# Performance work log

Hardware: AMD Instinct MI355X
Metric: run time of the kernel (lower is better)

Reference implementation:

```python
import jax, jax.numpy as jnp
import numpy as np

NUM_HEADS = 12
WINDOW = 128
LOOK_B = 1
LOOK_F = 1


def look_around(x, pad_value):
    # x: (b, n_windows, window, ...) ; pad along window axis (axis=1), concat along axis=2
    pads = [(0, 0), (LOOK_B, LOOK_F)] + [(0, 0)] * (x.ndim - 2)
    p = jnp.pad(x, pads, constant_values=pad_value)
    n = x.shape[1]
    return jnp.concatenate([p[:, i:i + n] for i in range(LOOK_B + LOOK_F + 1)], axis=2)


def split_heads(x):
    # (L, B, D) -> (B*H, L, hd), batch-major over heads (index = b*H + h)
    L, B, D = x.shape
    return jnp.transpose(x.reshape(L, B * NUM_HEADS, D // NUM_HEADS), (1, 0, 2))


def merge_heads(x):
    # (B*H, L, hd) -> (L, B, D)
    BH, L, hd = x.shape
    return jnp.transpose(x, (1, 0, 2)).reshape(L, BH // NUM_HEADS, hd * NUM_HEADS)


def setup_inputs() -> dict:
    key = jax.random.key(0)
    ks = jax.random.split(key, 12)
    S, B, D = 4096, 8, 768
    inp = {
        'hidden_states': jax.random.normal(ks[0], (S, B, D), dtype=jnp.float32),
        'key_padding_mask': jax.random.bernoulli(ks[1], 0.2, (B, S)),
    }
    scale = 0.02
    for i, name in enumerate(['Wq', 'Wk', 'Wv', 'Wgq']):
        inp[name] = jax.random.normal(ks[2 + i], (D, D), dtype=jnp.float32) * scale
    for i, name in enumerate(['bq', 'bk', 'bv', 'bgq']):
        inp[name] = jax.random.normal(ks[6 + i], (D,), dtype=jnp.float32) * scale
    return inp


def reference(hidden_states, key_padding_mask, Wq, bq, Wk, bk, Wv, bv, Wgq, bgq):
    S, B, D = hidden_states.shape
    H, W = NUM_HEADS, WINDOW
    hd = D // H
    n = S // W
    BH = B * H
    neg = -jnp.finfo(hidden_states.dtype).max
    inv_sqrt = hd ** (-0.5)

    q = split_heads(hidden_states @ Wq + bq)  # (BH, S, hd)
    k = split_heads(hidden_states @ Wk + bk)
    v = split_heads(hidden_states @ Wv + bv)

    # --- local windowed attention ---
    bq_ = q.reshape(BH, n, W, hd)
    bk_ = look_around(k.reshape(BH, n, W, hd), 0.0)   # (BH, n, 3W, hd)
    bv_ = look_around(v.reshape(BH, n, W, hd), 0.0)
    dots = jnp.einsum('bnie,bnje->bnij', bq_, bk_) * inv_sqrt  # (BH, n, W, 3W)

    im = key_padding_mask.reshape(B, n, W)
    km = look_around(im, True)                        # (B, n, 3W), pads masked
    mask = im[:, :, :, None] | km[:, :, None, :]      # (B, n, W, 3W)
    mask = jnp.broadcast_to(mask[:, None], (B, H, n, W, 3 * W)).reshape(BH, n, W, 3 * W)
    dots = jnp.where(mask, neg, dots)
    attn = jax.nn.softmax(dots, axis=-1)
    out = jnp.einsum('bnij,bnje->bnie', attn, bv_).reshape(BH, S, hd)
    out = merge_heads(out)                            # (S, B, D)

    # --- global-token attention (token 0 attends to everything) ---
    gq = split_heads(hidden_states[0:1] @ Wgq + bgq)  # (BH, 1, hd)
    gdots = jnp.einsum('bie,bje->bij', gq, k) * inv_sqrt  # (BH, 1, S)
    gmask = jnp.broadcast_to(key_padding_mask[:, None], (B, H, S)).reshape(BH, S)
    gdots = jnp.where(gmask[:, None, :], neg, gdots)
    gattn = jax.nn.softmax(gdots, axis=-1)
    gout = merge_heads(jnp.einsum('bij,bje->bie', gattn, v))  # (1, B, D)

    return out.at[0].set(gout[0])
```

## Files before the change

### kernel.cpp

```cpp
#include <hip/hip_runtime.h>
#include <float.h>

#define S_  4096
#define B_  8
#define D_  768
#define H_  12
#define HD_ 64
#define W_  128
#define BH_ 96
#define SB_ 32768

typedef unsigned short u16;
typedef __attribute__((ext_vector_type(8))) short bf16x8;
typedef __attribute__((ext_vector_type(4))) float f32x4;

#define MFMA16(a,b,c) __builtin_amdgcn_mfma_f32_16x16x32_bf16(a,b,c,0,0,0)

__device__ __forceinline__ u16 f2bf(float x){
  unsigned int u = __float_as_uint(x);
  return (u16)((u + 0x7FFFu + ((u >> 16) & 1u)) >> 16);
}
__device__ __forceinline__ float bf2f(unsigned int lo16){ return __uint_as_float(lo16 << 16); }
__device__ __forceinline__ float bflo(unsigned int u){ return __uint_as_float(u << 16); }
__device__ __forceinline__ float bfhi(unsigned int u){ return __uint_as_float(u & 0xFFFF0000u); }
__device__ __forceinline__ unsigned int pk2(float a, float b){
  return (unsigned int)f2bf(a) | ((unsigned int)f2bf(b) << 16);
}

__device__ __forceinline__ bool mask_at(const void* mp, int flag, int idx){
  return flag ? (((const unsigned char*)mp)[idx] != 0)
              : (((const unsigned int*)mp)[idx] != 0u);
}

__global__ __launch_bounds__(256) void sniff_mask_kernel(const unsigned int* __restrict__ m,
                                                         int* __restrict__ flag){
  __shared__ unsigned int red[256];
  unsigned int acc = 0u;
  for (int i = threadIdx.x; i < 8192; i += 256) acc |= m[i];
  red[threadIdx.x] = acc;
  __syncthreads();
  for (int s = 128; s > 0; s >>= 1){
    if ((int)threadIdx.x < s) red[threadIdx.x] |= red[threadIdx.x + s];
    __syncthreads();
  }
  if (threadIdx.x == 0){
    unsigned int o = red[0];
    *flag = (o > 1u && (o & 0xFEFEFEFEu) == 0u) ? 1 : 0;
  }
}

__global__ __launch_bounds__(256) void cvt_hidden_kernel(const float* __restrict__ src,
                                                         u16* __restrict__ dst){
  int idx = blockIdx.x * 256 + threadIdx.x;
  for (int base = idx * 8; base < 25165824; base += 2048 * 256 * 8){
    float4 a = *(const float4*)&src[base];
    float4 b = *(const float4*)&src[base + 4];
    uint4 o;
    o.x = pk2(a.x, a.y); o.y = pk2(a.z, a.w);
    o.z = pk2(b.x, b.y); o.w = pk2(b.z, b.w);
    *(uint4*)&dst[base] = o;
  }
}

__global__ __launch_bounds__(256) void cvt_wT_kernel(const float* __restrict__ W0,
    const float* __restrict__ W1, const float* __restrict__ W2, u16* __restrict__ wT){
  __shared__ float tile[64][65];
  const float* Wsel = blockIdx.z == 0 ? W0 : (blockIdx.z == 1 ? W1 : W2);
  const int t = threadIdx.x;
  const int kt0 = blockIdx.x * 64, nt0 = blockIdx.y * 64;
  { const int row = t >> 2, c16 = (t & 3) * 16;
#pragma unroll
    for (int j = 0; j < 4; ++j){
      float4 v = *(const float4*)&Wsel[(size_t)(kt0 + row) * 768 + nt0 + c16 + j * 4];
      tile[row][c16 + j*4 + 0] = v.x; tile[row][c16 + j*4 + 1] = v.y;
      tile[row][c16 + j*4 + 2] = v.z; tile[row][c16 + j*4 + 3] = v.w;
    } }
  __syncthreads();
  { const int nl = t >> 2, k16 = (t & 3) * 16;
    unsigned int o[8];
#pragma unroll
    for (int j = 0; j < 8; ++j)
      o[j] = pk2(tile[k16 + 2*j][nl], tile[k16 + 2*j + 1][nl]);
    u16* dst = wT + (size_t)blockIdx.z * 589824 + (size_t)(nt0 + nl) * 768 + kt0 + k16;
    *(uint4*)dst       = make_uint4(o[0], o[1], o[2], o[3]);
    *(uint4*)(dst + 8) = make_uint4(o[4], o[5], o[6], o[7]); }
}

__global__ __launch_bounds__(256) void proj_mfma_kernel(
    const u16* __restrict__ hb, const u16* __restrict__ wT,
    const float* __restrict__ bq, const float* __restrict__ bk, const float* __restrict__ bv,
    u16* __restrict__ qb, u16* __restrict__ kb, u16* __restrict__ vb){
  __shared__ u16 As[128][72];
  __shared__ u16 Bs[128][72];
  const int t = threadIdx.x;
  const int p  = blockIdx.y / 6;
  const int c0 = (blockIdx.y % 6) * 128;
  const int r0 = blockIdx.x * 128;
  const float* bias = p == 0 ? bq : (p == 1 ? bk : bv);
  u16* dst = p == 0 ? qb : (p == 1 ? kb : vb);
  const u16* wTp = wT + (size_t)p * 589824;

  const int lane = t & 63, w = t >> 6;
  const int l15 = lane & 15, lg = lane >> 4;
  const int wr = w >> 1, wc = w & 1;

  f32x4 acc[4][4] = {};

  for (int k0 = 0; k0 < 768; k0 += 64){
#pragma unroll
    for (int i = 0; i < 4; ++i){
      int chunk = i * 256 + t;
      int row = chunk >> 3, q8 = (chunk & 7) * 8;
      *(uint4*)&As[row][q8] = *(const uint4*)&hb[(size_t)(r0 + row) * 768 + k0 + q8];
      *(uint4*)&Bs[row][q8] = *(const uint4*)&wTp[(size_t)(c0 + row) * 768 + k0 + q8];
    }
    __syncthreads();
    bf16x8 af[4][2], bf[4][2];
#pragma unroll
    for (int mf = 0; mf < 4; ++mf)
#pragma unroll
      for (int ks = 0; ks < 2; ++ks)
        af[mf][ks] = *(const bf16x8*)&As[wr*64 + mf*16 + l15][ks*32 + lg*8];
#pragma unroll
    for (int nf = 0; nf < 4; ++nf)
#pragma unroll
      for (int ks = 0; ks < 2; ++ks)
        bf[nf][ks] = *(const bf16x8*)&Bs[wc*64 + nf*16 + l15][ks*32 + lg*8];
#pragma unroll
    for (int ks = 0; ks < 2; ++ks)
#pragma unroll
      for (int mf = 0; mf < 4; ++mf)
#pragma unroll
        for (int nf = 0; nf < 4; ++nf)
          acc[mf][nf] = MFMA16(af[mf][ks], bf[nf][ks], acc[mf][nf]);
    __syncthreads();
  }
#pragma unroll
  for (int nf = 0; nf < 4; ++nf){
    int c = c0 + wc*64 + nf*16 + l15;
    float bsv = bias[c];
    int hh = c >> 6, dd = c & 63;
#pragma unroll
    for (int mf = 0; mf < 4; ++mf){
      int rbase = r0 + wr*64 + mf*16 + lg*4;
#pragma unroll
      for (int r = 0; r < 4; ++r){
        int row = rbase + r;
        int s = row >> 3, b = row & 7;
        dst[((size_t)(b * 12 + hh) * 4096 + s) * 64 + dd] = f2bf(acc[mf][nf][r] + bsv);
      }
    }
  }
}

__global__ __launch_bounds__(256) void vt_kernel(const u16* __restrict__ vb, u16* __restrict__ vtb){
  __shared__ u16 tile[64][72];
  const int t = threadIdx.x;
  const int stile = blockIdx.x, bh = blockIdx.y;
  { const int sl = t >> 2, q = (t & 3) * 16;
    const u16* src = &vb[((size_t)bh * 4096 + stile * 64 + sl) * 64 + q];
    *(uint4*)&tile[sl][q]     = *(const uint4*)src;
    *(uint4*)&tile[sl][q + 8] = *(const uint4*)(src + 8); }
  __syncthreads();
  { const int d = t >> 2, sq = (t & 3) * 16;
    unsigned int o[8];
#pragma unroll
    for (int j = 0; j < 8; ++j){
      unsigned int lo = tile[sq + 2*j][d], hi = tile[sq + 2*j + 1][d];
      o[j] = lo | (hi << 16);
    }
    u16* dst = vtb + ((size_t)bh * 64 + d) * 4096 + stile * 64 + sq;
    *(uint4*)dst       = make_uint4(o[0], o[1], o[2], o[3]);
    *(uint4*)(dst + 8) = make_uint4(o[4], o[5], o[6], o[7]); }
}

__global__ __launch_bounds__(256) void local_mfma_kernel(
    const u16* __restrict__ qb, const u16* __restrict__ kb, const u16* __restrict__ vtb,
    const void* __restrict__ maskp, const int* __restrict__ flagp,
    float* __restrict__ out){
  __shared__ u16 Ks[64][72];
  __shared__ u16 Vs[64][72];
  __shared__ u16 Ps[4][32][72];
  __shared__ float kpen[384];
  __shared__ float qpen_s[128];
  const int t = threadIdx.x;
  const int n_i = blockIdx.x, bh = blockIdx.y;
  const int b_i = bh / 12, h = bh % 12;
  const int flag = *flagp;
  const int w = t >> 6, lane = t & 63, l15 = lane & 15, lg = lane >> 4;
  const int jbase0 = n_i * 128 - 128;

  if (t < 128) qpen_s[t] = mask_at(maskp, flag, b_i * 4096 + n_i * 128 + t) ? 1.f : 0.f;
  for (int j = t; j < 384; j += 256){
    int jp = jbase0 + j;
    kpen[j] = (jp < 0 || jp >= 4096 || mask_at(maskp, flag, b_i * 4096 + jp)) ? 1.f : 0.f;
  }
  __syncthreads();

  bf16x8 aq[2][2];
#pragma unroll
  for (int mf = 0; mf < 2; ++mf)
#pragma unroll
    for (int ks = 0; ks < 2; ++ks)
      aq[mf][ks] = *(const bf16x8*)&qb[((size_t)bh * 4096 + n_i*128 + w*32 + mf*16 + l15) * 64 + ks*32 + lg*8];

  float qp[2][4];
#pragma unroll
  for (int mf = 0; mf < 2; ++mf)
#pragma unroll
    for (int r = 0; r < 4; ++r)
      qp[mf][r] = qpen_s[w*32 + mf*16 + lg*4 + r];

  f32x4 O[2][4] = {};
  float mrow[2][4], lrow[2][4];
#pragma unroll
  for (int mf = 0; mf < 2; ++mf)
#pragma unroll
    for (int r = 0; r < 4; ++r){ mrow[mf][r] = -FLT_MAX; lrow[mf][r] = 0.f; }

  for (int jt = 0; jt < 6; ++jt){
    const int jb = jbase0 + jt * 64;
    if (jb < 0 || jb >= 4096) continue;
#pragma unroll
    for (int i = 0; i < 2; ++i){
      int chunk = i * 256 + t;
      int row = chunk >> 3, q8 = (chunk & 7) * 8;
      *(uint4*)&Ks[row][q8] = *(const uint4*)&kb[((size_t)bh * 4096 + jb + row) * 64 + q8];
      *(uint4*)&Vs[row][q8] = *(const uint4*)&vtb[((size_t)bh * 64 + row) * 4096 + jb + q8];
    }
    __syncthreads();

    f32x4 dt[2][4] = {};
#pragma unroll
    for (int ks = 0; ks < 2; ++ks)
#pragma unroll
      for (int nf = 0; nf < 4; ++nf){
        bf16x8 bk_ = *(const bf16x8*)&Ks[nf*16 + l15][ks*32 + lg*8];
        dt[0][nf] = MFMA16(aq[0][ks], bk_, dt[0][nf]);
        dt[1][nf] = MFMA16(aq[1][ks], bk_, dt[1][nf]);
      }
#pragma unroll
    for (int nf = 0; nf < 4; ++nf){
      float kp = kpen[jt*64 + nf*16 + l15];
#pragma unroll
      for (int mf = 0; mf < 2; ++mf)
#pragma unroll
        for (int r = 0; r < 4; ++r){
          float vv = dt[mf][nf][r] * 0.125f;
          dt[mf][nf][r] = (qp[mf][r] + kp == 0.f) ? vv : -FLT_MAX;
        }
    }
#pragma unroll
    for (int mf = 0; mf < 2; ++mf)
#pragma unroll
      for (int r = 0; r < 4; ++r){
        float tm = fmaxf(fmaxf(dt[mf][0][r], dt[mf][1][r]), fmaxf(dt[mf][2][r], dt[mf][3][r]));
        tm = fmaxf(tm, __shfl_xor(tm, 1));
        tm = fmaxf(tm, __shfl_xor(tm, 2));
        tm = fmaxf(tm, __shfl_xor(tm, 4));
        tm = fmaxf(tm, __shfl_xor(tm, 8));
        float mold = mrow[mf][r];
        float mnew = fmaxf(mold, tm);
        float scl = __expf(mold - mnew);
        mrow[mf][r] = mnew;
        float ps = 0.f;
#pragma unroll
        for (int nf = 0; nf < 4; ++nf){
          float pv = __expf(dt[mf][nf][r] - mnew);
          ps += pv;
          Ps[w][mf*16 + lg*4 + r][nf*16 + l15] = f2bf(pv);
          O[mf][nf][r] *= scl;
        }
        ps += __shfl_xor(ps, 1);
        ps += __shfl_xor(ps, 2);
        ps += __shfl_xor(ps, 4);
        ps += __shfl_xor(ps, 8);
        lrow[mf][r] = lrow[mf][r] * scl + ps;
      }
#pragma unroll
    for (int ks = 0; ks < 2; ++ks){
      bf16x8 ap0 = *(const bf16x8*)&Ps[w][l15]     [ks*32 + lg*8];
      bf16x8 ap1 = *(const bf16x8*)&Ps[w][16 + l15][ks*32 + lg*8];
#pragma unroll
      for (int nf = 0; nf < 4; ++nf){
        bf16x8 bv_ = *(const bf16x8*)&Vs[nf*16 + l15][ks*32 + lg*8];
        O[0][nf] = MFMA16(ap0, bv_, O[0][nf]);
        O[1][nf] = MFMA16(ap1, bv_, O[1][nf]);
      }
    }
    __syncthreads();
  }

  const float noor = (n_i == 0 || n_i == 31) ? 128.f : 0.f;
#pragma unroll
  for (int mf = 0; mf < 2; ++mf)
#pragma unroll
    for (int r = 0; r < 4; ++r){
      float lf = lrow[mf][r] + ((mrow[mf][r] <= -FLT_MAX) ? noor : 0.f);
      float inv = 1.f / lf;
      int srow = n_i*128 + w*32 + mf*16 + lg*4 + r;
      float* op = &out[(size_t)srow * (8 * 768) + b_i * 768 + h * 64];
#pragma unroll
      for (int nf = 0; nf < 4; ++nf)
        op[nf*16 + l15] = O[mf][nf][r] * inv;
    }
}

__global__ __launch_bounds__(256) void gq_kernel(const float* __restrict__ hid,
    const float* __restrict__ Wgq, const float* __restrict__ bgq, float* __restrict__ gq){
  __shared__ float hs[768];
  __shared__ float red[256];
  const int t = threadIdx.x, bh = blockIdx.x, b_i = bh / 12, h = bh % 12;
  for (int c = t; c < 768; c += 256) hs[c] = hid[(size_t)b_i * 768 + c];
  __syncthreads();
  const int dd = t & 63, part = t >> 6;
  float acc = 0.f;
  for (int c = part * 192; c < part * 192 + 192; ++c)
    acc += hs[c] * Wgq[(size_t)c * 768 + h * 64 + dd];
  red[t] = acc;
  __syncthreads();
  if (t < 64)
    gq[bh * 64 + t] = (red[t] + red[t+64] + red[t+128] + red[t+192] + bgq[h*64 + t]) * 0.125f;
}

__global__ __launch_bounds__(256) void gpart_kernel(const float* __restrict__ gq,
    const u16* __restrict__ kb, const u16* __restrict__ vb,
    const void* __restrict__ maskp, const int* __restrict__ flagp,
    float* __restrict__ gp_out){
  __shared__ float gqs[64];
  __shared__ float sc[512];
  __shared__ float red[256];
  const int t = threadIdx.x, bh = blockIdx.x, chunk = blockIdx.y;
  const int b_i = bh / 12;
  const int flag = *flagp;
  if (t < 64) gqs[t] = gq[bh * 64 + t];
  __syncthreads();
#pragma unroll
  for (int i = 0; i < 2; ++i){
    int sl = i * 256 + t;
    int s = chunk * 512 + sl;
    const uint4* kr = (const uint4*)&kb[((size_t)bh * 4096 + s) * 64];
    float dot = 0.f;
#pragma unroll
    for (int u = 0; u < 8; ++u){
      uint4 x = kr[u];
      dot += gqs[u*8+0]*bflo(x.x) + gqs[u*8+1]*bfhi(x.x);
      dot += gqs[u*8+2]*bflo(x.y) + gqs[u*8+3]*bfhi(x.y);
      dot += gqs[u*8+4]*bflo(x.z) + gqs[u*8+5]*bfhi(x.z);
      dot += gqs[u*8+6]*bflo(x.w) + gqs[u*8+7]*bfhi(x.w);
    }
    sc[sl] = mask_at(maskp, flag, b_i * 4096 + s) ? -FLT_MAX : dot;
  }
  __syncthreads();
  float m = fmaxf(sc[t], sc[t + 256]);
  red[t] = m; __syncthreads();
  for (int st = 128; st > 0; st >>= 1){ if (t < st) red[t] = fmaxf(red[t], red[t + st]); __syncthreads(); }
  const float mc = red[0];
  __syncthreads();
  float ls = 0.f;
#pragma unroll
  for (int i = 0; i < 2; ++i){
    int sl = i * 256 + t;
    float p = __expf(sc[sl] - mc);
    sc[sl] = p; ls += p;
  }
  red[t] = ls; __syncthreads();
  for (int st = 128; st > 0; st >>= 1){ if (t < st) red[t] += red[t + st]; __syncthreads(); }
  const float lc = red[0];
  __syncthreads();
  const int dd = t & 63, part = t >> 6;
  float o = 0.f;
  for (int i2 = 0; i2 < 128; ++i2){
    int sl = part * 128 + i2;
    o += sc[sl] * bf2f(vb[((size_t)bh * 4096 + chunk * 512 + sl) * 64 + dd]);
  }
  red[t] = o; __syncthreads();
  float* gp = gp_out + ((size_t)bh * 8 + chunk) * 66;
  if (t == 0){ gp[0] = mc; gp[1] = lc; }
  if (t < 64) gp[2 + t] = red[t] + red[t+64] + red[t+128] + red[t+192];
}

__global__ __launch_bounds__(64) void greduce_kernel(const float* __restrict__ gp_in,
                                                     float* __restrict__ out){
  const int t = threadIdx.x, bh = blockIdx.x, b_i = bh / 12, h = bh % 12;
  const float* gp = gp_in + (size_t)bh * 8 * 66;
  float mg = -FLT_MAX;
#pragma unroll
  for (int c = 0; c < 8; ++c) mg = fmaxf(mg, gp[c * 66]);
  float lg = 0.f, o = 0.f;
#pragma unroll
  for (int c = 0; c < 8; ++c){
    float wv = __expf(gp[c * 66] - mg);
    lg += gp[c * 66 + 1] * wv;
    o  += gp[c * 66 + 2 + t] * wv;
  }
  out[(size_t)b_i * 768 + h * 64 + t] = o / lg;
}

extern "C" void kernel_launch(void* const* d_in, const int* in_sizes, int n_in,
                              void* d_out, int out_size, void* d_ws, size_t ws_size,
                              hipStream_t stream) {
  const float* hid   = (const float*)d_in[0];
  const void*  maskp = d_in[1];
  const float* Wq  = (const float*)d_in[2];
  const float* Wk  = (const float*)d_in[3];
  const float* Wv  = (const float*)d_in[4];
  const float* Wgq = (const float*)d_in[5];
  const float* bq  = (const float*)d_in[6];
  const float* bk  = (const float*)d_in[7];
  const float* bv  = (const float*)d_in[8];
  const float* bgq = (const float*)d_in[9];
  float* out = (float*)d_out;

  char* wsb = (char*)d_ws;
  int* flag   = (int*)wsb;
  u16* hb     = (u16*)(wsb + 256);
  u16* wT     = (u16*)(wsb + 50331904);
  u16* qb     = (u16*)(wsb + 53870848);
  u16* kb     = (u16*)(wsb + 104202496);
  u16* vb     = (u16*)(wsb + 154534144);
  u16* vtb    = (u16*)(wsb + 204865792);
  float* gq   = (float*)(wsb + 255197440);
  float* gpart = (float*)(wsb + 255222016);

  sniff_mask_kernel<<<1, 256, 0, stream>>>((const unsigned int*)maskp, flag);
  cvt_hidden_kernel<<<2048, 256, 0, stream>>>(hid, hb);
  cvt_wT_kernel<<<dim3(12, 12, 3), 256, 0, stream>>>(Wq, Wk, Wv, wT);
  proj_mfma_kernel<<<dim3(256, 18), 256, 0, stream>>>(hb, wT, bq, bk, bv, qb, kb, vb);
  vt_kernel<<<dim3(64, 96), 256, 0, stream>>>(vb, vtb);
  gq_kernel<<<96, 256, 0, stream>>>(hid, Wgq, bgq, gq);
  local_mfma_kernel<<<dim3(32, 96), 256, 0, stream>>>(qb, kb, vtb, maskp, flag, out);
  gpart_kernel<<<dim3(96, 8), 256, 0, stream>>>(gq, kb, vb, maskp, flag, gpart);
  greduce_kernel<<<96, 64, 0, stream>>>(gpart, out);
}
```

Baseline: 431.2 us.

## Use direct global-to-LDS loads with XOR swizzle, XCD block remap, and MFMA priority

In the projection GEMM and the local attention kernel, global-to-LDS tile staging now goes through global_load_lds, which skips the round trip through registers. The padded shared-memory arrays are replaced by unpadded tiles with an XOR swizzle on the 16-byte slot index to avoid bank conflicts. The launch grid is flattened and block IDs are remapped so that consecutive IDs (id&7) are spread across the chiplet XCDs, aiming for better L2 locality. s_setprio is raised around the MFMA sections of the attention loop. The swizzle indexing has to match exactly between the writes and the reads, and the LDS-direct loads depend on each wave's lane-to-address layout.

```diff
diff --git a/kernel.cpp b/kernel.cpp
--- a/kernel.cpp
+++ b/kernel.cpp
@@ -25,6 +25,12 @@
 __device__ __forceinline__ float bfhi(unsigned int u){ return __uint_as_float(u & 0xFFFF0000u); }
 __device__ __forceinline__ unsigned int pk2(float a, float b){
   return (unsigned int)f2bf(a) | ((unsigned int)f2bf(b) << 16);
+}
+
+__device__ __forceinline__ void gload_lds16(const void* g, void* l){
+  __builtin_amdgcn_global_load_lds(
+      (const __attribute__((address_space(1))) void*)g,
+      (__attribute__((address_space(3))) void*)l, 16, 0, 0);
 }
 
 __device__ __forceinline__ bool mask_at(const void* mp, int flag, int idx){
@@ -90,12 +96,15 @@
     const u16* __restrict__ hb, const u16* __restrict__ wT,
     const float* __restrict__ bq, const float* __restrict__ bk, const float* __restrict__ bv,
     u16* __restrict__ qb, u16* __restrict__ kb, u16* __restrict__ vb){
-  __shared__ u16 As[128][72];
-  __shared__ u16 Bs[128][72];
+  __shared__ u16 As[128 * 64];
+  __shared__ u16 Bs[128 * 64];
   const int t = threadIdx.x;
-  const int p  = blockIdx.y / 6;
-  const int c0 = (blockIdx.y % 6) * 128;
-  const int r0 = blockIdx.x * 128;
+  const int id = blockIdx.x;
+  const int swz = (id & 7) * 576 + (id >> 3);
+  const int mt = swz & 255, nt = swz >> 8;
+  const int p  = nt / 6;
+  const int c0 = (nt % 6) * 128;
+  const int r0 = mt * 128;
   const float* bias = p == 0 ? bq : (p == 1 ? bk : bv);
   u16* dst = p == 0 ? qb : (p == 1 ? kb : vb);
   const u16* wTp = wT + (size_t)p * 589824;
@@ -103,16 +112,18 @@
   const int lane = t & 63, w = t >> 6;
   const int l15 = lane & 15, lg = lane >> 4;
   const int wr = w >> 1, wc = w & 1;
+  const int lrc = lane >> 3, slot = lane & 7;
 
   f32x4 acc[4][4] = {};
 
   for (int k0 = 0; k0 < 768; k0 += 64){
 #pragma unroll
-    for (int i = 0; i < 4; ++i){
-      int chunk = i * 256 + t;
-      int row = chunk >> 3, q8 = (chunk & 7) * 8;
-      *(uint4*)&As[row][q8] = *(const uint4*)&hb[(size_t)(r0 + row) * 768 + k0 + q8];
-      *(uint4*)&Bs[row][q8] = *(const uint4*)&wTp[(size_t)(c0 + row) * 768 + k0 + q8];
+    for (int c = 0; c < 4; ++c){
+      int chunk = w * 4 + c;
+      int ldsrow = chunk * 8 + lrc;
+      int slotg = slot ^ (ldsrow & 7);
+      gload_lds16(&hb [(size_t)(r0 + ldsrow) * 768 + k0 + slotg * 8], &As[chunk * 512]);
+      gload_lds16(&wTp[(size_t)(c0 + ldsrow) * 768 + k0 + slotg * 8], &Bs[chunk * 512]);
     }
     __syncthreads();
     bf16x8 af[4][2], bf[4][2];
@@ -120,12 +131,12 @@
     for (int mf = 0; mf < 4; ++mf)
 #pragma unroll
       for (int ks = 0; ks < 2; ++ks)
-        af[mf][ks] = *(const bf16x8*)&As[wr*64 + mf*16 + l15][ks*32 + lg*8];
+        af[mf][ks] = *(const bf16x8*)&As[(wr*64 + mf*16 + l15) * 64 + (((ks*4 + lg) ^ (l15 & 7)) * 8)];
 #pragma unroll
     for (int nf = 0; nf < 4; ++nf)
 #pragma unroll
       for (int ks = 0; ks < 2; ++ks)
-        bf[nf][ks] = *(const bf16x8*)&Bs[wc*64 + nf*16 + l15][ks*32 + lg*8];
+        bf[nf][ks] = *(const bf16x8*)&Bs[(wc*64 + nf*16 + l15) * 64 + (((ks*4 + lg) ^ (l15 & 7)) * 8)];
 #pragma unroll
     for (int ks = 0; ks < 2; ++ks)
 #pragma unroll
@@ -178,16 +189,19 @@
     const u16* __restrict__ qb, const u16* __restrict__ kb, const u16* __restrict__ vtb,
     const void* __restrict__ maskp, const int* __restrict__ flagp,
     float* __restrict__ out){
-  __shared__ u16 Ks[64][72];
-  __shared__ u16 Vs[64][72];
+  __shared__ u16 Ks[64 * 64];
+  __shared__ u16 Vs[64 * 64];
   __shared__ u16 Ps[4][32][72];
   __shared__ float kpen[384];
   __shared__ float qpen_s[128];
   const int t = threadIdx.x;
-  const int n_i = blockIdx.x, bh = blockIdx.y;
+  const int id = blockIdx.x;
+  const int swz = (id & 7) * 384 + (id >> 3);
+  const int n_i = swz & 31, bh = swz >> 5;
   const int b_i = bh / 12, h = bh % 12;
   const int flag = *flagp;
   const int w = t >> 6, lane = t & 63, l15 = lane & 15, lg = lane >> 4;
+  const int lrc = lane >> 3, slot = lane & 7;
   const int jbase0 = n_i * 128 - 128;
 
   if (t < 128) qpen_s[t] = mask_at(maskp, flag, b_i * 4096 + n_i * 128 + t) ? 1.f : 0.f;
@@ -222,23 +236,26 @@
     const int jb = jbase0 + jt * 64;
     if (jb < 0 || jb >= 4096) continue;
 #pragma unroll
-    for (int i = 0; i < 2; ++i){
-      int chunk = i * 256 + t;
-      int row = chunk >> 3, q8 = (chunk & 7) * 8;
-      *(uint4*)&Ks[row][q8] = *(const uint4*)&kb[((size_t)bh * 4096 + jb + row) * 64 + q8];
-      *(uint4*)&Vs[row][q8] = *(const uint4*)&vtb[((size_t)bh * 64 + row) * 4096 + jb + q8];
+    for (int c = 0; c < 2; ++c){
+      int chunk = w * 2 + c;
+      int ldsrow = chunk * 8 + lrc;
+      int slotg = slot ^ (ldsrow & 7);
+      gload_lds16(&kb [((size_t)bh * 4096 + jb + ldsrow) * 64 + slotg * 8], &Ks[chunk * 512]);
+      gload_lds16(&vtb[((size_t)bh * 64 + ldsrow) * 4096 + jb + slotg * 8], &Vs[chunk * 512]);
     }
     __syncthreads();
 
     f32x4 dt[2][4] = {};
+    __builtin_amdgcn_s_setprio(1);
 #pragma unroll
     for (int ks = 0; ks < 2; ++ks)
 #pragma unroll
       for (int nf = 0; nf < 4; ++nf){
-        bf16x8 bk_ = *(const bf16x8*)&Ks[nf*16 + l15][ks*32 + lg*8];
+        bf16x8 bk_ = *(const bf16x8*)&Ks[(nf*16 + l15) * 64 + (((ks*4 + lg) ^ (l15 & 7)) * 8)];
         dt[0][nf] = MFMA16(aq[0][ks], bk_, dt[0][nf]);
         dt[1][nf] = MFMA16(aq[1][ks], bk_, dt[1][nf]);
       }
+    __builtin_amdgcn_s_setprio(0);
 #pragma unroll
     for (int nf = 0; nf < 4; ++nf){
       float kp = kpen[jt*64 + nf*16 + l15];
@@ -277,17 +294,19 @@
         ps += __shfl_xor(ps, 8);
         lrow[mf][r] = lrow[mf][r] * scl + ps;
       }
+    __builtin_amdgcn_s_setprio(1);
 #pragma unroll
     for (int ks = 0; ks < 2; ++ks){
       bf16x8 ap0 = *(const bf16x8*)&Ps[w][l15]     [ks*32 + lg*8];
       bf16x8 ap1 = *(const bf16x8*)&Ps[w][16 + l15][ks*32 + lg*8];
 #pragma unroll
       for (int nf = 0; nf < 4; ++nf){
-        bf16x8 bv_ = *(const bf16x8*)&Vs[nf*16 + l15][ks*32 + lg*8];
+        bf16x8 bv_ = *(const bf16x8*)&Vs[(nf*16 + l15) * 64 + (((ks*4 + lg) ^ (l15 & 7)) * 8)];
         O[0][nf] = MFMA16(ap0, bv_, O[0][nf]);
         O[1][nf] = MFMA16(ap1, bv_, O[1][nf]);
       }
     }
+    __builtin_amdgcn_s_setprio(0);
     __syncthreads();
   }
 
@@ -426,10 +445,10 @@
   sniff_mask_kernel<<<1, 256, 0, stream>>>((const unsigned int*)maskp, flag);
   cvt_hidden_kernel<<<2048, 256, 0, stream>>>(hid, hb);
   cvt_wT_kernel<<<dim3(12, 12, 3), 256, 0, stream>>>(Wq, Wk, Wv, wT);
-  proj_mfma_kernel<<<dim3(256, 18), 256, 0, stream>>>(hb, wT, bq, bk, bv, qb, kb, vb);
+  proj_mfma_kernel<<<4608, 256, 0, stream>>>(hb, wT, bq, bk, bv, qb, kb, vb);
   vt_kernel<<<dim3(64, 96), 256, 0, stream>>>(vb, vtb);
   gq_kernel<<<96, 256, 0, stream>>>(hid, Wgq, bgq, gq);
-  local_mfma_kernel<<<dim3(32, 96), 256, 0, stream>>>(qb, kb, vtb, maskp, flag, out);
+  local_mfma_kernel<<<3072, 256, 0, stream>>>(qb, kb, vtb, maskp, flag, out);
   gpart_kernel<<<dim3(96, 8), 256, 0, stream>>>(gq, kb, vb, maskp, flag, gpart);
   greduce_kernel<<<96, 64, 0, stream>>>(gpart, out);
 }
```

Result: no change. 438.0 us (+1.6%).
